# Kernel optimization log

Measured on AMD Instinct MI355X. Metric: run time of the kernel, lower is better.

The kernel has to match this reference:

```python
import jax, jax.numpy as jnp
import numpy as np

NX = 320   # image matrix (nRead)
NC = 8     # coils
NT = 8     # motion states
M = 65536  # non-Cartesian k-space samples per frame
OS = 2     # gridding oversampling factor


def setup_inputs() -> dict:
    key = jax.random.key(0)
    ks = jax.random.split(key, 7)
    kspace_r = jax.random.normal(ks[0], (NC, M), jnp.float32)
    kspace_i = jax.random.normal(ks[1], (NC, M), jnp.float32)
    # k-space trajectory normalized to [-0.5, 0.5)
    traj = jax.random.uniform(ks[2], (M, 2, NT), jnp.float32, -0.5, 0.5)
    csm_r = jax.random.normal(ks[3], (NC, NX, NX), jnp.float32)
    csm_i = jax.random.normal(ks[4], (NC, NX, NX), jnp.float32)
    dcf = jax.random.uniform(ks[5], (M, NT), jnp.float32)
    # motion/flow field in pixels, [NX, NX, 2, NT]
    motions = 3.0 * jax.random.normal(ks[6], (NX, NX, 2, NT), jnp.float32)
    return dict(kspace_r=kspace_r, kspace_i=kspace_i, traj=traj,
                csm_r=csm_r, csm_i=csm_i, dcf=dcf, motions=motions)


def _grid_adjoint(kspace, traj_t, dcf_t, csm):
    """Adjoint NUFFT (gpuNUFFT adj_op): density-compensated bilinear gridding
    onto a 2x oversampled Cartesian grid, inverse FFT, center crop,
    deapodization, and conjugate coil combination."""
    G = OS * NX
    data = (kspace * dcf_t[None, :]).astype(jnp.complex64)  # [NC, M]
    u = (traj_t[:, 0] + 0.5) * G
    v = (traj_t[:, 1] + 0.5) * G
    u0 = jnp.floor(u)
    v0 = jnp.floor(v)
    du = (u - u0).astype(jnp.float32)
    dv = (v - v0).astype(jnp.float32)
    i0 = u0.astype(jnp.int32) % G
    i1 = (i0 + 1) % G
    j0 = v0.astype(jnp.int32) % G
    j1 = (j0 + 1) % G
    grid = jnp.zeros((NC, G, G), jnp.complex64)
    grid = grid.at[:, i0, j0].add(data * ((1.0 - du) * (1.0 - dv)))
    grid = grid.at[:, i1, j0].add(data * (du * (1.0 - dv)))
    grid = grid.at[:, i0, j1].add(data * ((1.0 - du) * dv))
    grid = grid.at[:, i1, j1].add(data * (du * dv))
    im_os = jnp.fft.fftshift(
        jnp.fft.ifft2(jnp.fft.ifftshift(grid, axes=(-2, -1)), axes=(-2, -1)),
        axes=(-2, -1))
    s = (G - NX) // 2
    im = im_os[:, s:s + NX, s:s + NX]  # [NC, NX, NX]
    # deapodization: FT of the triangle (bilinear) gridding kernel is sinc^2
    x = (jnp.arange(NX, dtype=jnp.float32) - NX // 2) / G
    d = jnp.sinc(x) ** 2
    im = im / (d[:, None] * d[None, :])
    # conjugate coil combine with sensitivity maps
    return jnp.sum(jnp.conj(csm) * im, axis=0).astype(jnp.complex64)


def _bilinear_warp(im, flow):
    """apply_sparse_motion: sparse bilinear-interpolation warp of a 2D image
    by a per-pixel displacement field flow[..., 0:2] (in pixels)."""
    Nx, Ny = im.shape
    xs = jnp.arange(Nx, dtype=jnp.float32)[:, None] + flow[..., 0]
    ys = jnp.arange(Ny, dtype=jnp.float32)[None, :] + flow[..., 1]
    xs = jnp.clip(xs, 0.0, Nx - 1.0)
    ys = jnp.clip(ys, 0.0, Ny - 1.0)
    x0 = jnp.floor(xs).astype(jnp.int32)
    y0 = jnp.floor(ys).astype(jnp.int32)
    x1 = jnp.minimum(x0 + 1, Nx - 1)
    y1 = jnp.minimum(y0 + 1, Ny - 1)
    dx = xs - x0.astype(jnp.float32)
    dy = ys - y0.astype(jnp.float32)
    return ((1.0 - dx) * (1.0 - dy) * im[x0, y0]
            + dx * (1.0 - dy) * im[x1, y0]
            + (1.0 - dx) * dy * im[x0, y1]
            + dx * dy * im[x1, y1])


def reference(kspace_r, kspace_i, traj, csm_r, csm_i, dcf, motions):
    kspace = (kspace_r + 1j * kspace_i).astype(jnp.complex64)
    csm = (csm_r + 1j * csm_i).astype(jnp.complex64)

    def frame(traj_t, dcf_t, flow_t):
        im = _grid_adjoint(kspace, traj_t, dcf_t, csm)
        return _bilinear_warp(im, flow_t)

    # vmap over motion states: traj[..., t], dcf[..., t], motions[..., t]
    per_frame = jax.vmap(frame, in_axes=(2, 1, 3))(traj, dcf, motions)  # [NT, NX, NX]
    out = jnp.sum(per_frame, axis=0)  # temporal sum, complex [NX, NX]
    return jnp.stack([out.real, out.imag], axis=-1)  # [NX, NX, 2]
```

## Files before the change

kernel.cpp:

```cpp
#include <hip/hip_runtime.h>
#include <math.h>

#define NXI 320
#define NCI 8
#define NTI 8
#define MI  65536
#define GI  640
#define G2I (GI*GI)
#define NPIX (NXI*NXI)
#define REC_F 20
#define NBINS (NTI*G2I)
#define SCAN_BLKS2 (NBINS/4096)

typedef float v2f __attribute__((ext_vector_type(2)));

__device__ inline v2f cmul(v2f a, v2f b) {
    v2f axx = __builtin_shufflevector(a, a, 0, 0);
    v2f ayy = __builtin_shufflevector(a, a, 1, 1);
    v2f byx = __builtin_shufflevector(b, b, 1, 0);
    v2f r = axx * b;
    v2f t = ayy * byx;
    return r + v2f{-t.x, t.y};
}

template<int H>
__device__ inline float sxf(float x) {
    if constexpr (H == 1) {
        return __int_as_float(__builtin_amdgcn_update_dpp(
            __float_as_int(x), __float_as_int(x), 0xB1, 0xF, 0xF, false));
    } else if constexpr (H == 2) {
        return __int_as_float(__builtin_amdgcn_update_dpp(
            __float_as_int(x), __float_as_int(x), 0x4E, 0xF, 0xF, false));
    } else if constexpr (H == 8) {
        return __int_as_float(__builtin_amdgcn_update_dpp(
            __float_as_int(x), __float_as_int(x), 0x128, 0xF, 0xF, false));
    } else {
        return __shfl_xor(x, H, 64);
    }
}
template<int H>
__device__ inline v2f sxv(v2f v) { return v2f{sxf<H>(v.x), sxf<H>(v.y)}; }

__device__ inline void cell_of(const float* __restrict__ traj, int m, int f,
                               int& i0s, int& j0s, float& du, float& dv)
{
    float tu = traj[(m*2 + 0)*NTI + f];
    float tv = traj[(m*2 + 1)*NTI + f];
    float u = (tu + 0.5f) * (float)GI;
    float v = (tv + 0.5f) * (float)GI;
    float fu = floorf(u), fv = floorf(v);
    du = u - fu; dv = v - fv;
    i0s = (int)fu + GI/2; if (i0s >= GI) i0s -= GI;
    j0s = (int)fv + GI/2; if (j0s >= GI) j0s -= GI;
}

__global__ __launch_bounds__(256) void count_cells(
    const float* __restrict__ traj, int* __restrict__ counts)
{
    int tid = blockIdx.x * 256 + threadIdx.x;
    int f = tid >> 16, m = tid & (MI - 1);
    int i0s, j0s; float du, dv;
    cell_of(traj, m, f, i0s, j0s, du, dv);
    atomicAdd(&counts[f*G2I + i0s*GI + j0s], 1);
}

__device__ inline int wave_incl_scan(int v, int lane) {
    #pragma unroll
    for (int d = 1; d < 64; d <<= 1) {
        int y = __shfl_up(v, d, 64);
        if (lane >= d) v += y;
    }
    return v;
}

__global__ __launch_bounds__(1024) void scanA(const int4* __restrict__ counts4,
                                              int4* __restrict__ binstart4,
                                              int* __restrict__ sums)
{
    __shared__ int wtot[16];
    int tid = threadIdx.x, lane = tid & 63, wv = tid >> 6;
    int i = blockIdx.x * 1024 + tid;
    int4 c = counts4[i];
    int s = c.x + c.y + c.z + c.w;
    int incl = wave_incl_scan(s, lane);
    if (lane == 63) wtot[wv] = incl;
    __syncthreads();
    if (wv == 0 && lane < 16) {
        int t = wtot[lane];
        #pragma unroll
        for (int d = 1; d < 16; d <<= 1) {
            int y = __shfl_up(t, d, 64);
            if (lane >= d) t += y;
        }
        wtot[lane] = t;
    }
    __syncthreads();
    int woff = wv ? wtot[wv - 1] : 0;
    int excl = woff + incl - s;
    int4 b;
    b.x = excl; b.y = excl + c.x; b.z = b.y + c.y; b.w = b.z + c.z;
    binstart4[i] = b;
    if (tid == 1023) sums[blockIdx.x] = woff + incl;
}

__global__ __launch_bounds__(1024) void scanB(int* __restrict__ sums,
                                              int* __restrict__ binstart)
{
    __shared__ int tmp[1024];
    int tid = threadIdx.x;
    int v = (tid < SCAN_BLKS2) ? sums[tid] : 0;
    tmp[tid] = v; __syncthreads();
    for (int d = 1; d < 1024; d <<= 1) {
        int y = (tid >= d) ? tmp[tid - d] : 0;
        __syncthreads();
        tmp[tid] += y;
        __syncthreads();
    }
    int incl = tmp[tid];
    if (tid < SCAN_BLKS2) sums[tid] = incl - v;
    if (tid == SCAN_BLKS2 - 1) {
        sums[SCAN_BLKS2] = incl;
        binstart[NBINS] = 0;
    }
}

__global__ __launch_bounds__(256) void scatter_cells(
    const float* __restrict__ kr, const float* __restrict__ ki,
    const float* __restrict__ traj, const float* __restrict__ dcf,
    int* __restrict__ counts, const int* __restrict__ binstart,
    const int* __restrict__ sums, float* __restrict__ recs)
{
    int tid = blockIdx.x * 256 + threadIdx.x;
    int f = tid >> 16, m = tid & (MI - 1);
    int i0s, j0s; float du, dv;
    cell_of(traj, m, f, i0s, j0s, du, dv);
    float w = dcf[m*NTI + f];
    int bin = f*G2I + i0s*GI + j0s;
    int within = atomicSub(&counts[bin], 1) - 1;
    int slot = binstart[bin] + sums[bin >> 12] + within;
    float4* r = (float4*)(recs + (size_t)slot * REC_F);
    r[0] = make_float4(du, 1.f - du, dv, 1.f - dv);
    #pragma unroll
    for (int q = 0; q < 4; ++q) {
        int c0 = 2*q;
        r[1+q] = make_float4(kr[c0*MI + m]*w,     ki[c0*MI + m]*w,
                             kr[(c0+1)*MI + m]*w, ki[(c0+1)*MI + m]*w);
    }
}

__device__ inline void dft5p(v2f x0, v2f x1, v2f x2, v2f x3, v2f x4, v2f* X)
{
    const float c1 = 0.309016994f, c2 = -0.809016994f;
    const float s1 = 0.951056516f, s2 =  0.587785252f;
    v2f S1 = x1 + x4, D1 = x1 - x4;
    v2f S2 = x2 + x3, D2 = x2 - x3;
    X[0] = x0 + S1 + S2;
    v2f A = x0 + c1*S1 + c2*S2;
    v2f T = s1*D1 + s2*D2;
    v2f B = x0 + c2*S1 + c1*S2;
    v2f U = s2*D1 - s1*D2;
    v2f iT = v2f{-T.y, T.x};
    v2f iU = v2f{-U.y, U.x};
    X[1] = A + iT;  X[4] = A - iT;
    X[2] = B + iU;  X[3] = B - iU;
}

template<int H, int S>
__device__ inline void bf_stage(v2f* a, int lane)
{
    const float PI = 3.14159265358979f;
    bool low = (lane & H) == 0;
    int kp = (lane << S) & 31;
    float sn, cs;
    __sincosf((2.0f * PI / 64.0f) * (float)kp, &sn, &cs);
    v2f w = low ? v2f{1.f, 0.f} : v2f{cs, sn};
    float sg = low ? 1.f : -1.f;
    v2f sgv = v2f{sg, sg};
    #pragma unroll
    for (int n = 0; n < 10; ++n) {
        v2f p = sxv<H>(a[n]);
        v2f t = sgv * a[n] + p;
        a[n] = cmul(t, w);
    }
}

__device__ inline void fft640_pruned(v2f* a, int lane, v2f* line, int xorm)
{
    const float PI = 3.14159265358979f;
    bf_stage<32, 0>(a, lane);
    bf_stage<16, 1>(a, lane);
    bf_stage< 8, 2>(a, lane);
    bf_stage< 4, 3>(a, lane);
    bf_stage< 2, 4>(a, lane);
    bf_stage< 1, 5>(a, lane);
    int k1 = __brev(lane) >> 26;
    float th2 = (2.0f * PI / 640.0f) * (float)k1;
    float sn, cs;
    __sincosf(th2, &sn, &cs);
    v2f wb = v2f{cs, sn};
    v2f w = wb;
    #pragma unroll
    for (int n = 1; n < 10; ++n) {
        a[n] = cmul(a[n], w);
        w = cmul(w, wb);
    }
    v2f E[5], O[5];
    dft5p(a[0], a[2], a[4], a[6], a[8], E);
    dft5p(a[1], a[3], a[5], a[7], a[9], O);
    const v2f tk1 = { 0.809016994f, 0.587785252f};
    const v2f tk2 = { 0.309016994f, 0.951056516f};
    const v2f tk3 = {-0.309016994f, 0.951056516f};
    const v2f tk4 = {-0.809016994f, 0.587785252f};
    v2f t1 = cmul(tk1, O[1]);
    v2f t2 = cmul(tk2, O[2]);
    v2f t3 = cmul(tk3, O[3]);
    v2f t4 = cmul(tk4, O[4]);
    bool hi = (k1 >= 32);
    line[(160 + k1) ^ xorm] = E[0] + O[0];
    line[(224 + k1) ^ xorm] = E[1] + t1;
    int yx = hi ? (k1 - 32) : (288 + k1);
    v2f zx = hi ? (E[2] - t2) : (E[2] + t2);
    line[yx ^ xorm] = zx;
    line[(32 + k1) ^ xorm] = E[3] - t3;
    line[(96 + k1) ^ xorm] = E[4] - t4;
}

__global__ __launch_bounds__(512, 8) void row_fft(
    const int* __restrict__ binstart, const int* __restrict__ sums,
    const float* __restrict__ recs, v2f* __restrict__ rowout)
{
    __shared__ v2f A[NCI][GI];
    int bid = blockIdx.x;
    int i = bid % GI;
    int f = bid / GI;
    int tid = threadIdx.x;
    int im1 = i ? i - 1 : GI - 1;
    const int base0 = f*G2I + i*GI;
    const int base1 = f*G2I + im1*GI;

    #define GS(b) (binstart[b] + sums[(b) >> 12])

    for (int j = tid; j < GI; j += 512) {
        v2f acc[NCI];
        #pragma unroll
        for (int c = 0; c < NCI; ++c) acc[c] = v2f{0.f, 0.f};
        #pragma unroll
        for (int p = 0; p < 2; ++p) {
            const int base = p ? base1 : base0;
            if (j > 0) {
                int lo = GS(base + j - 1), mid = GS(base + j), hi = GS(base + j + 1);
                for (int s = lo; s < hi; ++s) {
                    const float4* R = (const float4*)(recs + (size_t)s*REC_F);
                    float4 h4 = R[0];
                    float wr = p ? h4.x : h4.y;
                    float w  = wr * ((s < mid) ? h4.z : h4.w);
                    float4 d0 = R[1], d1 = R[2], d2 = R[3], d3 = R[4];
                    acc[0] += w * v2f{d0.x, d0.y};  acc[1] += w * v2f{d0.z, d0.w};
                    acc[2] += w * v2f{d1.x, d1.y};  acc[3] += w * v2f{d1.z, d1.w};
                    acc[4] += w * v2f{d2.x, d2.y};  acc[5] += w * v2f{d2.z, d2.w};
                    acc[6] += w * v2f{d3.x, d3.y};  acc[7] += w * v2f{d3.z, d3.w};
                }
            } else {
                #pragma unroll
                for (int side = 0; side < 2; ++side) {
                    int b = base + (side ? 0 : (GI - 1));
                    int s0 = GS(b), s1 = GS(b + 1);
                    for (int s = s0; s < s1; ++s) {
                        const float4* R = (const float4*)(recs + (size_t)s*REC_F);
                        float4 h4 = R[0];
                        float wr = p ? h4.x : h4.y;
                        float w  = wr * (side ? h4.w : h4.z);
                        float4 d0 = R[1], d1 = R[2], d2 = R[3], d3 = R[4];
                        acc[0] += w * v2f{d0.x, d0.y};  acc[1] += w * v2f{d0.z, d0.w};
                        acc[2] += w * v2f{d1.x, d1.y};  acc[3] += w * v2f{d1.z, d1.w};
                        acc[4] += w * v2f{d2.x, d2.y};  acc[5] += w * v2f{d2.z, d2.w};
                        acc[6] += w * v2f{d3.x, d3.y};  acc[7] += w * v2f{d3.z, d3.w};
                    }
                }
            }
        }
        #pragma unroll
        for (int c = 0; c < NCI; ++c) A[c][j] = acc[c];
    }
    #undef GS
    __syncthreads();

    int wv = tid >> 6, lane = tid & 63;
    v2f a[10];
    #pragma unroll
    for (int n = 0; n < 10; ++n) a[n] = A[wv][10*lane + n];
    fft640_pruned(a, lane, A[wv], 0);
    v2f* dst = rowout + (((size_t)f*NCI + wv)*GI + i)*NXI;
    #pragma unroll
    for (int q = 0; q < 5; ++q) {
        int yc = lane + 64*q;
        dst[yc] = A[wv][yc];
    }
}

__global__ __launch_bounds__(512, 8) void col_fft_combine(
    const v2f* __restrict__ rowout, const float* __restrict__ csr,
    const float* __restrict__ csi, float* __restrict__ img)
{
    __shared__ v2f A[8][GI];
    int bid = blockIdx.x;
    int g = bid % 40;
    int c = (bid / 40) % NCI;
    int f = bid / (40*NCI);
    int y0 = g * 8;
    int tid = threadIdx.x;
    const v2f* src = rowout + ((size_t)f*NCI + c)*GI*NXI + y0;
    for (int idx = tid; idx < 8*GI; idx += 512) {
        int l = idx & 7, k = idx >> 3;
        A[l][k ^ (4*(l & 3))] = src[(size_t)k*NXI + l];
    }
    __syncthreads();
    int wv = tid >> 6, lane = tid & 63;
    int xm = 4 * (wv & 3);
    v2f a[10];
    #pragma unroll
    for (int n = 0; n < 10; ++n) a[n] = A[wv][(10*lane + n) ^ xm];
    fft640_pruned(a, lane, A[wv], xm);
    __syncthreads();
    float* imgf = img + (size_t)f * NPIX * 2;
    for (int idx = tid; idx < 8*NXI; idx += 512) {
        int l = idx & 7, xx = idx >> 3;
        v2f gv = A[l][xx ^ (4*(l & 3))];
        int pix = xx*NXI + y0 + l;
        float cr = csr[c*NPIX + pix];
        float ci = csi[c*NPIX + pix];
        atomicAdd(&imgf[2*pix + 0], cr*gv.x + ci*gv.y);
        atomicAdd(&imgf[2*pix + 1], cr*gv.y - ci*gv.x);
    }
}

__global__ __launch_bounds__(320) void deapod_init(float* __restrict__ dinv)
{
    int x = threadIdx.x;
    const float PI = 3.14159265358979f;
    float t = (x - 160) * (1.0f/GI);
    float d = 1.0f;
    if (x != 160) { float s = __sinf(PI*t) / (PI*t); d = s*s; }
    dinv[x] = (1.0f/GI) / d;
}

__global__ __launch_bounds__(256) void warp_sum(
    const float2* __restrict__ img, const float* __restrict__ motions,
    const float* __restrict__ dinv, float* __restrict__ out)
{
    int pix = blockIdx.x * 256 + threadIdx.x;
    int x = pix / NXI, y = pix - x*NXI;
    float accr = 0.f, acci = 0.f;
    #pragma unroll
    for (int f = 0; f < NTI; ++f) {
        float fx = motions[(size_t)(pix*2 + 0)*NTI + f];
        float fy = motions[(size_t)(pix*2 + 1)*NTI + f];
        float xs = fminf(fmaxf((float)x + fx, 0.0f), (float)(NXI-1));
        float ys = fminf(fmaxf((float)y + fy, 0.0f), (float)(NXI-1));
        int x0 = (int)floorf(xs);
        int y0 = (int)floorf(ys);
        int x1 = min(x0+1, NXI-1);
        int y1 = min(y0+1, NXI-1);
        float dx = xs - (float)x0;
        float dy = ys - (float)y0;
        float ax0 = dinv[x0], ax1 = dinv[x1];
        float ay0 = dinv[y0], ay1 = dinv[y1];
        const float2* im = img + (size_t)f*NPIX;
        float2 v00 = im[x0*NXI + y0];
        float2 v10 = im[x1*NXI + y0];
        float2 v01 = im[x0*NXI + y1];
        float2 v11 = im[x1*NXI + y1];
        float w00 = (1.f-dx)*(1.f-dy)*ax0*ay0, w10 = dx*(1.f-dy)*ax1*ay0;
        float w01 = (1.f-dx)*dy*ax0*ay1,       w11 = dx*dy*ax1*ay1;
        accr += w00*v00.x + w10*v10.x + w01*v01.x + w11*v11.x;
        acci += w00*v00.y + w10*v10.y + w01*v01.y + w11*v11.y;
    }
    out[pix*2+0] = accr;
    out[pix*2+1] = acci;
}

extern "C" void kernel_launch(void* const* d_in, const int* in_sizes, int n_in,
                              void* d_out, int out_size, void* d_ws, size_t ws_size,
                              hipStream_t stream)
{
    const float* kr   = (const float*)d_in[0];
    const float* ki   = (const float*)d_in[1];
    const float* traj = (const float*)d_in[2];
    const float* csr  = (const float*)d_in[3];
    const float* csi  = (const float*)d_in[4];
    const float* dcf  = (const float*)d_in[5];
    const float* mot  = (const float*)d_in[6];
    float* out = (float*)d_out;

    char* ws = (char*)d_ws;
    float*  recs     = (float*)ws;
    ws += (size_t)NTI * MI * REC_F * sizeof(float);
    v2f*    rowout   = (v2f*)ws;
    ws += (size_t)NTI * NCI * GI * NXI * sizeof(float2);
    float2* img      = (float2*)ws;
    ws += (size_t)NTI * NPIX * sizeof(float2);
    int*    counts   = (int*)ws;  ws += (size_t)NBINS * sizeof(int);
    int*    binstart = (int*)ws;  ws += ((size_t)NBINS + 16) * sizeof(int);
    int*    sums     = (int*)ws;  ws += 16384;
    float*  dinv     = (float*)ws; ws += 512 * sizeof(float);

    hipMemsetAsync(counts, 0, (size_t)NBINS * sizeof(int), stream);
    hipMemsetAsync(img, 0, (size_t)NTI * NPIX * sizeof(float2), stream);
    deapod_init  <<<1, 320, 0, stream>>>(dinv);
    count_cells  <<<NTI*MI/256, 256, 0, stream>>>(traj, counts);
    scanA        <<<SCAN_BLKS2, 1024, 0, stream>>>((const int4*)counts,
                                                   (int4*)binstart, sums);
    scanB        <<<1,          1024, 0, stream>>>(sums, binstart);
    scatter_cells<<<NTI*MI/256, 256, 0, stream>>>(kr, ki, traj, dcf, counts,
                                                  binstart, sums, recs);
    row_fft      <<<NTI*GI,     512, 0, stream>>>(binstart, sums, recs, rowout);
    col_fft_combine<<<NTI*NCI*40, 512, 0, stream>>>(rowout, csr, csi, (float*)img);
    warp_sum     <<<NPIX/256,   256, 0, stream>>>(img, mot, dinv, out);
}
```

Baseline: 339.0 us.

## Restructure column FFT so each block combines all coils without atomics

Each column-FFT block now handles one image column for one frame, with one wave per coil. Each wave reads its column straight from global memory into registers instead of staging it through a transposed LDS tile. The coil combine happens in-block against a new pixel-major packed CSM buffer, so each pixel gets one plain store instead of global atomics, and the image memset goes away. The trade-off is strided uncoalesced global reads (stride NXI) for the column loads, plus an extra pre-pass kernel to pack the CSM.

Result: faster. 306.9 us (-9.5%).

```diff
diff --git a/kernel.cpp b/kernel.cpp
--- a/kernel.cpp
+++ b/kernel.cpp
@@ -298,39 +298,50 @@
     }
 }
 
+__global__ __launch_bounds__(256) void csm_pack(
+    const float* __restrict__ csr, const float* __restrict__ csi,
+    float2* __restrict__ csmt)
+{
+    int pix = blockIdx.x * 256 + threadIdx.x;
+    #pragma unroll
+    for (int c = 0; c < NCI; ++c)
+        csmt[(size_t)pix*NCI + c] = make_float2(csr[c*NPIX + pix],
+                                                csi[c*NPIX + pix]);
+}
+
 __global__ __launch_bounds__(512, 8) void col_fft_combine(
-    const v2f* __restrict__ rowout, const float* __restrict__ csr,
-    const float* __restrict__ csi, float* __restrict__ img)
-{
-    __shared__ v2f A[8][GI];
+    const v2f* __restrict__ rowout, const float2* __restrict__ csmt,
+    float2* __restrict__ img)
+{
+    __shared__ v2f A[NCI][GI];
     int bid = blockIdx.x;
-    int g = bid % 40;
-    int c = (bid / 40) % NCI;
-    int f = bid / (40*NCI);
-    int y0 = g * 8;
+    int f = bid & 7;
+    int y = bid >> 3;
     int tid = threadIdx.x;
-    const v2f* src = rowout + ((size_t)f*NCI + c)*GI*NXI + y0;
-    for (int idx = tid; idx < 8*GI; idx += 512) {
-        int l = idx & 7, k = idx >> 3;
-        A[l][k ^ (4*(l & 3))] = src[(size_t)k*NXI + l];
-    }
+    int wv = tid >> 6, lane = tid & 63;
+
+    const v2f* src = rowout + ((size_t)(f*NCI + wv)*GI)*NXI + y;
+    v2f a[10];
+    #pragma unroll
+    for (int n = 0; n < 10; ++n) a[n] = src[(size_t)(10*lane + n)*NXI];
+    fft640_pruned(a, lane, A[wv], 0);
     __syncthreads();
-    int wv = tid >> 6, lane = tid & 63;
-    int xm = 4 * (wv & 3);
-    v2f a[10];
-    #pragma unroll
-    for (int n = 0; n < 10; ++n) a[n] = A[wv][(10*lane + n) ^ xm];
-    fft640_pruned(a, lane, A[wv], xm);
-    __syncthreads();
-    float* imgf = img + (size_t)f * NPIX * 2;
-    for (int idx = tid; idx < 8*NXI; idx += 512) {
-        int l = idx & 7, xx = idx >> 3;
-        v2f gv = A[l][xx ^ (4*(l & 3))];
-        int pix = xx*NXI + y0 + l;
-        float cr = csr[c*NPIX + pix];
-        float ci = csi[c*NPIX + pix];
-        atomicAdd(&imgf[2*pix + 0], cr*gv.x + ci*gv.y);
-        atomicAdd(&imgf[2*pix + 1], cr*gv.y - ci*gv.x);
+
+    if (tid < NXI) {
+        int x = tid;
+        const float4* cs = (const float4*)(csmt + ((size_t)x*NXI + y)*NCI);
+        float4 c01 = cs[0], c23 = cs[1], c45 = cs[2], c67 = cs[3];
+        float accr = 0.f, acci = 0.f;
+        v2f g;
+        g = A[0][x]; accr += c01.x*g.x + c01.y*g.y; acci += c01.x*g.y - c01.y*g.x;
+        g = A[1][x]; accr += c01.z*g.x + c01.w*g.y; acci += c01.z*g.y - c01.w*g.x;
+        g = A[2][x]; accr += c23.x*g.x + c23.y*g.y; acci += c23.x*g.y - c23.y*g.x;
+        g = A[3][x]; accr += c23.z*g.x + c23.w*g.y; acci += c23.z*g.y - c23.w*g.x;
+        g = A[4][x]; accr += c45.x*g.x + c45.y*g.y; acci += c45.x*g.y - c45.y*g.x;
+        g = A[5][x]; accr += c45.z*g.x + c45.w*g.y; acci += c45.z*g.y - c45.w*g.x;
+        g = A[6][x]; accr += c67.x*g.x + c67.y*g.y; acci += c67.x*g.y - c67.y*g.x;
+        g = A[7][x]; accr += c67.z*g.x + c67.w*g.y; acci += c67.z*g.y - c67.w*g.x;
+        img[(size_t)f*NPIX + x*NXI + y] = make_float2(accr, acci);
     }
 }
 
@@ -399,14 +410,16 @@
     ws += (size_t)NTI * NCI * GI * NXI * sizeof(float2);
     float2* img      = (float2*)ws;
     ws += (size_t)NTI * NPIX * sizeof(float2);
+    float2* csmt     = (float2*)ws;
+    ws += (size_t)NPIX * NCI * sizeof(float2);
     int*    counts   = (int*)ws;  ws += (size_t)NBINS * sizeof(int);
     int*    binstart = (int*)ws;  ws += ((size_t)NBINS + 16) * sizeof(int);
     int*    sums     = (int*)ws;  ws += 16384;
     float*  dinv     = (float*)ws; ws += 512 * sizeof(float);
 
     hipMemsetAsync(counts, 0, (size_t)NBINS * sizeof(int), stream);
-    hipMemsetAsync(img, 0, (size_t)NTI * NPIX * sizeof(float2), stream);
     deapod_init  <<<1, 320, 0, stream>>>(dinv);
+    csm_pack     <<<NPIX/256, 256, 0, stream>>>(csr, csi, csmt);
     count_cells  <<<NTI*MI/256, 256, 0, stream>>>(traj, counts);
     scanA        <<<SCAN_BLKS2, 1024, 0, stream>>>((const int4*)counts,
                                                    (int4*)binstart, sums);
@@ -414,6 +427,6 @@
     scatter_cells<<<NTI*MI/256, 256, 0, stream>>>(kr, ki, traj, dcf, counts,
                                                   binstart, sums, recs);
     row_fft      <<<NTI*GI,     512, 0, stream>>>(binstart, sums, recs, rowout);
-    col_fft_combine<<<NTI*NCI*40, 512, 0, stream>>>(rowout, csr, csi, (float*)img);
+    col_fft_combine<<<NTI*NXI,  512, 0, stream>>>(rowout, csmt, img);
     warp_sum     <<<NPIX/256,   256, 0, stream>>>(img, mot, dinv, out);
 }
```

## Accumulate coils in registers in column FFT, fuse init and scan kernels

Applied to the files above, without the earlier changes.

The column FFT kernel now handles four coils per block and accumulates the coil-combined result in registers. It writes two partial images (one per coil half) instead of doing float atomics into a zeroed image, and warp_sum reads both halves. The coil maps are repacked into a coil-interleaved layout by a new init kernel, which also zeroes the counts and computes the deapodization table, replacing two memsets and a launch. ScanA and scanB are merged with a last-block-done pattern, which adds a global counter and fences. Occupancy bounds are relaxed, and the next coil's slab is prefetched into registers while the current one is processed.

After: 359.4 us. +6.0%, slower.

```diff
diff --git a/kernel.cpp b/kernel.cpp
--- a/kernel.cpp
+++ b/kernel.cpp
@@ -54,6 +54,29 @@
     j0s = (int)fv + GI/2; if (j0s >= GI) j0s -= GI;
 }
 
+__global__ __launch_bounds__(256) void init_pack(
+    const float* __restrict__ csr, const float* __restrict__ csi,
+    float2* __restrict__ csmt, int4* __restrict__ counts4,
+    float* __restrict__ dinv, int* __restrict__ done)
+{
+    int gid = blockIdx.x * 256 + threadIdx.x;
+    #pragma unroll
+    for (int c = 0; c < NCI; ++c)
+        csmt[(size_t)gid*NCI + c] = make_float2(csr[c*NPIX + gid],
+                                                csi[c*NPIX + gid]);
+    #pragma unroll
+    for (int k = 0; k < 8; ++k)
+        counts4[(size_t)k*NPIX + gid] = make_int4(0, 0, 0, 0);
+    if (gid < NXI) {
+        const float PI = 3.14159265358979f;
+        float t = (gid - 160) * (1.0f/GI);
+        float d = 1.0f;
+        if (gid != 160) { float s = __sinf(PI*t) / (PI*t); d = s*s; }
+        dinv[gid] = (1.0f/GI) / d;
+    }
+    if (gid == 0) *done = 0;
+}
+
 __global__ __launch_bounds__(256) void count_cells(
     const float* __restrict__ traj, int* __restrict__ counts)
 {
@@ -73,11 +96,14 @@
     return v;
 }
 
-__global__ __launch_bounds__(1024) void scanA(const int4* __restrict__ counts4,
-                                              int4* __restrict__ binstart4,
-                                              int* __restrict__ sums)
+__global__ __launch_bounds__(1024) void scanAB(const int4* __restrict__ counts4,
+                                               int4* __restrict__ binstart4,
+                                               int* __restrict__ sums,
+                                               int* __restrict__ done)
 {
     __shared__ int wtot[16];
+    __shared__ int tmp[1024];
+    __shared__ int isLast;
     int tid = threadIdx.x, lane = tid & 63, wv = tid >> 6;
     int i = blockIdx.x * 1024 + tid;
     int4 c = counts4[i];
@@ -100,27 +126,28 @@
     int4 b;
     b.x = excl; b.y = excl + c.x; b.z = b.y + c.y; b.w = b.z + c.z;
     binstart4[i] = b;
-    if (tid == 1023) sums[blockIdx.x] = woff + incl;
-}
-
-__global__ __launch_bounds__(1024) void scanB(int* __restrict__ sums,
-                                              int* __restrict__ binstart)
-{
-    __shared__ int tmp[1024];
-    int tid = threadIdx.x;
-    int v = (tid < SCAN_BLKS2) ? sums[tid] : 0;
-    tmp[tid] = v; __syncthreads();
-    for (int d = 1; d < 1024; d <<= 1) {
-        int y = (tid >= d) ? tmp[tid - d] : 0;
-        __syncthreads();
-        tmp[tid] += y;
-        __syncthreads();
-    }
-    int incl = tmp[tid];
-    if (tid < SCAN_BLKS2) sums[tid] = incl - v;
-    if (tid == SCAN_BLKS2 - 1) {
-        sums[SCAN_BLKS2] = incl;
-        binstart[NBINS] = 0;
+    if (tid == 1023) {
+        sums[blockIdx.x] = woff + incl;
+        __threadfence();
+        isLast = (atomicAdd(done, 1) == SCAN_BLKS2 - 1);
+    }
+    __syncthreads();
+    if (isLast) {
+        __threadfence();
+        int v = (tid < SCAN_BLKS2) ? atomicAdd(&sums[tid], 0) : 0;
+        tmp[tid] = v; __syncthreads();
+        for (int d = 1; d < 1024; d <<= 1) {
+            int y = (tid >= d) ? tmp[tid - d] : 0;
+            __syncthreads();
+            tmp[tid] += y;
+            __syncthreads();
+        }
+        int incl2 = tmp[tid];
+        if (tid < SCAN_BLKS2) sums[tid] = incl2 - v;
+        if (tid == SCAN_BLKS2 - 1) {
+            sums[SCAN_BLKS2] = incl2;
+            ((int*)binstart4)[NBINS] = 0;
+        }
     }
 }
 
@@ -298,54 +325,80 @@
     }
 }
 
-__global__ __launch_bounds__(512, 8) void col_fft_combine(
-    const v2f* __restrict__ rowout, const float* __restrict__ csr,
-    const float* __restrict__ csi, float* __restrict__ img)
+__global__ __launch_bounds__(512, 4) void col_fft_combine(
+    const v2f* __restrict__ rowout, const float2* __restrict__ csmt,
+    float2* __restrict__ img2)
 {
     __shared__ v2f A[8][GI];
     int bid = blockIdx.x;
-    int g = bid % 40;
-    int c = (bid / 40) % NCI;
-    int f = bid / (40*NCI);
-    int y0 = g * 8;
+    int f = bid & 7;
+    int r = bid >> 3;
+    int half = r & 1;
+    int yg = r >> 1;
+    int y0 = yg * 8;
+    int c0 = half * 4;
     int tid = threadIdx.x;
-    const v2f* src = rowout + ((size_t)f*NCI + c)*GI*NXI + y0;
-    for (int idx = tid; idx < 8*GI; idx += 512) {
-        int l = idx & 7, k = idx >> 3;
-        A[l][k ^ (4*(l & 3))] = src[(size_t)k*NXI + l];
-    }
-    __syncthreads();
     int wv = tid >> 6, lane = tid & 63;
-    int xm = 4 * (wv & 3);
-    v2f a[10];
-    #pragma unroll
-    for (int n = 0; n < 10; ++n) a[n] = A[wv][(10*lane + n) ^ xm];
-    fft640_pruned(a, lane, A[wv], xm);
-    __syncthreads();
-    float* imgf = img + (size_t)f * NPIX * 2;
-    for (int idx = tid; idx < 8*NXI; idx += 512) {
-        int l = idx & 7, xx = idx >> 3;
-        v2f gv = A[l][xx ^ (4*(l & 3))];
-        int pix = xx*NXI + y0 + l;
-        float cr = csr[c*NPIX + pix];
-        float ci = csi[c*NPIX + pix];
-        atomicAdd(&imgf[2*pix + 0], cr*gv.x + ci*gv.y);
-        atomicAdd(&imgf[2*pix + 1], cr*gv.y - ci*gv.x);
-    }
-}
-
-__global__ __launch_bounds__(320) void deapod_init(float* __restrict__ dinv)
-{
-    int x = threadIdx.x;
-    const float PI = 3.14159265358979f;
-    float t = (x - 160) * (1.0f/GI);
-    float d = 1.0f;
-    if (x != 160) { float s = __sinf(PI*t) / (PI*t); d = s*s; }
-    dinv[x] = (1.0f/GI) / d;
+
+    v2f acc[5];
+    #pragma unroll
+    for (int q = 0; q < 5; ++q) acc[q] = v2f{0.f, 0.f};
+
+    const size_t cstride = (size_t)GI * NXI;
+    const v2f* src = rowout + ((size_t)(f*NCI + c0)) * cstride + y0;
+    v2f L[10];
+    #pragma unroll
+    for (int t = 0; t < 10; ++t) {
+        int idx = tid + 512*t; int l = idx & 7, k = idx >> 3;
+        L[t] = src[(size_t)k*NXI + l];
+    }
+    #pragma unroll
+    for (int cc = 0; cc < 4; ++cc) {
+        #pragma unroll
+        for (int t = 0; t < 10; ++t) {
+            int idx = tid + 512*t; int l = idx & 7, k = idx >> 3;
+            A[l][k ^ (4*(l & 3))] = L[t];
+        }
+        if (cc < 3) {
+            const v2f* s2 = src + cstride * (cc + 1);
+            #pragma unroll
+            for (int t = 0; t < 10; ++t) {
+                int idx = tid + 512*t; int l = idx & 7, k = idx >> 3;
+                L[t] = s2[(size_t)k*NXI + l];
+            }
+        }
+        float2 cv[5];
+        #pragma unroll
+        for (int q = 0; q < 5; ++q) {
+            int P = tid + 512*q; int x = P >> 3, l = P & 7;
+            cv[q] = csmt[((size_t)x*NXI + y0 + l)*NCI + c0 + cc];
+        }
+        __syncthreads();
+        int xm = 4 * (wv & 3);
+        v2f a[10];
+        #pragma unroll
+        for (int n = 0; n < 10; ++n) a[n] = A[wv][(10*lane + n) ^ xm];
+        fft640_pruned(a, lane, A[wv], xm);
+        __syncthreads();
+        #pragma unroll
+        for (int q = 0; q < 5; ++q) {
+            int P = tid + 512*q; int x = P >> 3, l = P & 7;
+            v2f g = A[l][x ^ (4*(l & 3))];
+            acc[q].x += cv[q].x * g.x + cv[q].y * g.y;
+            acc[q].y += cv[q].x * g.y - cv[q].y * g.x;
+        }
+        __syncthreads();
+    }
+    float2* dst = img2 + ((size_t)half*NTI + f) * NPIX;
+    #pragma unroll
+    for (int q = 0; q < 5; ++q) {
+        int P = tid + 512*q; int x = P >> 3, l = P & 7;
+        dst[(size_t)x*NXI + y0 + l] = make_float2(acc[q].x, acc[q].y);
+    }
 }
 
 __global__ __launch_bounds__(256) void warp_sum(
-    const float2* __restrict__ img, const float* __restrict__ motions,
+    const float2* __restrict__ img2, const float* __restrict__ motions,
     const float* __restrict__ dinv, float* __restrict__ out)
 {
     int pix = blockIdx.x * 256 + threadIdx.x;
@@ -365,15 +418,18 @@
         float dy = ys - (float)y0;
         float ax0 = dinv[x0], ax1 = dinv[x1];
         float ay0 = dinv[y0], ay1 = dinv[y1];
-        const float2* im = img + (size_t)f*NPIX;
-        float2 v00 = im[x0*NXI + y0];
-        float2 v10 = im[x1*NXI + y0];
-        float2 v01 = im[x0*NXI + y1];
-        float2 v11 = im[x1*NXI + y1];
         float w00 = (1.f-dx)*(1.f-dy)*ax0*ay0, w10 = dx*(1.f-dy)*ax1*ay0;
         float w01 = (1.f-dx)*dy*ax0*ay1,       w11 = dx*dy*ax1*ay1;
-        accr += w00*v00.x + w10*v10.x + w01*v01.x + w11*v11.x;
-        acci += w00*v00.y + w10*v10.y + w01*v01.y + w11*v11.y;
+        #pragma unroll
+        for (int h = 0; h < 2; ++h) {
+            const float2* im = img2 + ((size_t)h*NTI + f)*NPIX;
+            float2 v00 = im[x0*NXI + y0];
+            float2 v10 = im[x1*NXI + y0];
+            float2 v01 = im[x0*NXI + y1];
+            float2 v11 = im[x1*NXI + y1];
+            accr += w00*v00.x + w10*v10.x + w01*v01.x + w11*v11.x;
+            acci += w00*v00.y + w10*v10.y + w01*v01.y + w11*v11.y;
+        }
     }
     out[pix*2+0] = accr;
     out[pix*2+1] = acci;
@@ -397,23 +453,24 @@
     ws += (size_t)NTI * MI * REC_F * sizeof(float);
     v2f*    rowout   = (v2f*)ws;
     ws += (size_t)NTI * NCI * GI * NXI * sizeof(float2);
-    float2* img      = (float2*)ws;
-    ws += (size_t)NTI * NPIX * sizeof(float2);
+    float2* img2     = (float2*)ws;
+    ws += (size_t)2 * NTI * NPIX * sizeof(float2);
+    float2* csmt     = (float2*)ws;
+    ws += (size_t)NPIX * NCI * sizeof(float2);
     int*    counts   = (int*)ws;  ws += (size_t)NBINS * sizeof(int);
     int*    binstart = (int*)ws;  ws += ((size_t)NBINS + 16) * sizeof(int);
     int*    sums     = (int*)ws;  ws += 16384;
     float*  dinv     = (float*)ws; ws += 512 * sizeof(float);
-
-    hipMemsetAsync(counts, 0, (size_t)NBINS * sizeof(int), stream);
-    hipMemsetAsync(img, 0, (size_t)NTI * NPIX * sizeof(float2), stream);
-    deapod_init  <<<1, 320, 0, stream>>>(dinv);
+    int*    done     = sums + 1024;
+
+    init_pack    <<<NPIX/256, 256, 0, stream>>>(csr, csi, csmt, (int4*)counts,
+                                                dinv, done);
     count_cells  <<<NTI*MI/256, 256, 0, stream>>>(traj, counts);
-    scanA        <<<SCAN_BLKS2, 1024, 0, stream>>>((const int4*)counts,
-                                                   (int4*)binstart, sums);
-    scanB        <<<1,          1024, 0, stream>>>(sums, binstart);
+    scanAB       <<<SCAN_BLKS2, 1024, 0, stream>>>((const int4*)counts,
+                                                   (int4*)binstart, sums, done);
     scatter_cells<<<NTI*MI/256, 256, 0, stream>>>(kr, ki, traj, dcf, counts,
                                                   binstart, sums, recs);
     row_fft      <<<NTI*GI,     512, 0, stream>>>(binstart, sums, recs, rowout);
-    col_fft_combine<<<NTI*NCI*40, 512, 0, stream>>>(rowout, csr, csi, (float*)img);
-    warp_sum     <<<NPIX/256,   256, 0, stream>>>(img, mot, dinv, out);
-}
+    col_fft_combine<<<NTI*NXI/4, 512, 0, stream>>>(rowout, csmt, img2);
+    warp_sum     <<<NPIX/256,   256, 0, stream>>>(img2, mot, dinv, out);
+}
```
